# Performance work log

Hardware: AMD Instinct MI355X
Metric: run time of the kernel (lower is better)

Reference implementation:

```python
import jax, jax.numpy as jnp
import numpy as np

K0 = 0.7978845608028654  # sqrt(2/pi)
C1 = 0.044715

def _gelu_tanh(x):
    # tanh-approx GELU, matching the Triton kernel's math
    return 0.5 * x * (1.0 + jnp.tanh(K0 * (x + C1 * x * x * x)))

def setup_inputs() -> dict:
    key = jax.random.key(0)
    k1, k2, k3 = jax.random.split(key, 3)
    B, C_in, H, W = 32, 64, 128, 128
    C_out, KH = 128, 3
    x = jax.random.normal(k1, (B, C_in, H, W), dtype=jnp.float32)
    weight = jax.random.normal(k2, (C_out, C_in, KH, KH), dtype=jnp.float32)
    bias = jax.random.normal(k3, (C_out,), dtype=jnp.float32)
    return {"x": x, "weight": weight, "bias": bias}

def reference(x, weight, bias):
    # Valid conv2d, stride 1 (NCHW, OIHW)
    y = jax.lax.conv_general_dilated(
        x, weight,
        window_strides=(1, 1), padding="VALID",
        dimension_numbers=("NCHW", "OIHW", "NCHW"))
    y = y + bias[None, :, None, None]
    y = _gelu_tanh(y)
    # global average pool over spatial dims -> [B, C_out]
    return jnp.mean(y, axis=(2, 3))
```

## Files before the change

### kernel.cpp

```cpp
#include <hip/hip_runtime.h>
#include <cstdint>
#include <cstddef>

#define GK0 0.7978845608028654f
#define GC1 0.044715f

typedef __attribute__((ext_vector_type(8))) short short8;
typedef __attribute__((ext_vector_type(4))) float floatx4;

__device__ __forceinline__ unsigned short f2bf(float f) {
  union { float f; unsigned int u; } v; v.f = f;
  unsigned int r = v.u + 0x7fffu + ((v.u >> 16) & 1u);
  return (unsigned short)(r >> 16);
}

__global__ void k_wt(const float* __restrict__ w, unsigned short* __restrict__ wt) {
  int t = blockIdx.x * 256 + threadIdx.x;
  if (t >= 128 * 64 * 9) return;
  int co = t / 576; int r = t - co * 576; int ci = r / 9; int khw = r - ci * 9;
  wt[(khw * 128 + co) * 64 + ci] = f2bf(w[t]);
}

__global__ void k_xt(const float* __restrict__ x, unsigned short* __restrict__ xb) {
  __shared__ float tile[128 * 65];
  int b = blockIdx.y, h = blockIdx.x;
  const float* src = x + ((size_t)b * 64 * 128 + h) * 128;
  for (int i = threadIdx.x; i < 64 * 128; i += 256) {
    int ci = i >> 7, w = i & 127;
    tile[w * 65 + ci] = src[(size_t)ci * 16384 + w];
  }
  __syncthreads();
  uint32_t* dst = (uint32_t*)(xb + (((size_t)b * 128 + h) * 128) * 64);
  for (int i = threadIdx.x; i < 128 * 32; i += 256) {
    int w = i >> 5, c2 = (i & 31) << 1;
    uint32_t u0 = f2bf(tile[w * 65 + c2]);
    uint32_t u1 = f2bf(tile[w * 65 + c2 + 1]);
    dst[i] = u0 | (u1 << 16);
  }
}

__global__ __launch_bounds__(256) void k_conv(
    const unsigned short* __restrict__ xb, const unsigned short* __restrict__ wt,
    const float* __restrict__ bias, float* __restrict__ out) {
  __shared__ unsigned short xs[4 * 66 * 72];
  const int tid = threadIdx.x;
  const int b = blockIdx.z, h0 = blockIdx.y * 2, w0 = blockIdx.x * 64;

  {
    const size_t base = (((size_t)b * 128 + h0) * 128) * 64;
    for (int t = tid; t < 2112; t += 256) {
      int hi = t / 528; int rem = t - hi * 528; int wi = rem >> 3; int c8 = (rem & 7) << 3;
      int wg = w0 + wi;
      int4 val = make_int4(0, 0, 0, 0);
      if (wg < 128) val = *(const int4*)(xb + base + ((size_t)hi * 128 + wg) * 64 + c8);
      *(int4*)(&xs[(hi * 66 + wi) * 72 + c8]) = val;
    }
  }
  __syncthreads();

  const int lane = tid & 63, wave = tid >> 6;
  const int wm = wave & 1, wn = wave >> 1;
  const int m = lane & 15, q = lane >> 4;

  floatx4 acc[4][4];
#pragma unroll
  for (int i = 0; i < 4; i++)
#pragma unroll
    for (int j = 0; j < 4; j++) acc[i][j] = (floatx4){0.f, 0.f, 0.f, 0.f};

  const unsigned short* wbase = wt + ((wm * 64 + m) * 64 + q * 8);
  int bb[4];
#pragma unroll
  for (int nt = 0; nt < 4; nt++) bb[nt] = (wn * 66 + nt * 16 + m) * 72 + q * 8;

  short8 a_cur[4], a_nxt[4];
#pragma unroll
  for (int mt = 0; mt < 4; mt++) a_cur[mt] = *(const short8*)(wbase + mt * 1024);

#pragma unroll
  for (int kk = 0; kk < 18; kk++) {
    const int khw = kk >> 1, cb = (kk & 1) << 5;
    const int kh = khw / 3, kw = khw - kh * 3;
    if (kk < 17) {
      const int khw2 = (kk + 1) >> 1, cb2 = ((kk + 1) & 1) << 5;
      const unsigned short* p = wbase + khw2 * 8192 + cb2;
#pragma unroll
      for (int mt = 0; mt < 4; mt++) a_nxt[mt] = *(const short8*)(p + mt * 1024);
    }
    short8 bf[4];
    const int off = (kh * 66 + kw) * 72 + cb;
#pragma unroll
    for (int nt = 0; nt < 4; nt++) bf[nt] = *(const short8*)(&xs[bb[nt] + off]);
#pragma unroll
    for (int mt = 0; mt < 4; mt++)
#pragma unroll
      for (int nt = 0; nt < 4; nt++)
        acc[mt][nt] = __builtin_amdgcn_mfma_f32_16x16x32_bf16(a_cur[mt], bf[nt], acc[mt][nt], 0, 0, 0);
#pragma unroll
    for (int mt = 0; mt < 4; mt++) a_cur[mt] = a_nxt[mt];
  }

  const float inv_area = 1.0f / (126.0f * 126.0f);
  float* orow = out + b * 128;
#pragma unroll
  for (int mt = 0; mt < 4; mt++) {
#pragma unroll
    for (int r = 0; r < 4; r++) {
      const int co = wm * 64 + mt * 16 + q * 4 + r;
      const float bv = bias[co];
      float s = 0.0f;
#pragma unroll
      for (int nt = 0; nt < 4; nt++) {
        float y = acc[mt][nt][r] + bv;
        float u = GK0 * (y + GC1 * y * y * y);
        float g = 0.5f * y * (1.0f + tanhf(u));
        if (w0 + nt * 16 + m < 126) s += g;
      }
#pragma unroll
      for (int d = 1; d < 16; d <<= 1) s += __shfl_xor(s, d, 64);
      if (m == 0) atomicAdd(&orow[co], s * inv_area);
    }
  }
}

extern "C" void kernel_launch(void* const* d_in, const int* in_sizes, int n_in,
                              void* d_out, int out_size, void* d_ws, size_t ws_size,
                              hipStream_t stream) {
  const float* x    = (const float*)d_in[0];
  const float* w    = (const float*)d_in[1];
  const float* bias = (const float*)d_in[2];
  float* out = (float*)d_out;

  unsigned short* xbuf = (unsigned short*)d_ws;
  unsigned short* wbuf = xbuf + (size_t)32 * 128 * 128 * 64;
  if (ws_size < (size_t)32 * 128 * 128 * 64 * 2 + 73728 * 2) return;

  hipMemsetAsync(d_out, 0, (size_t)out_size * sizeof(float), stream);
  k_wt<<<288, 256, 0, stream>>>(w, wbuf);
  k_xt<<<dim3(128, 32), 256, 0, stream>>>(x, xbuf);
  k_conv<<<dim3(2, 63, 32), 256, 0, stream>>>(xbuf, wbuf, bias, out);
}
```

Measured before the change: 434.9 us.

## Fuse fp32-to-bf16 input conversion into conv kernel, drop transpose pass

Removes the separate layout-transpose kernel and its bf16 workspace buffer; the conv kernel now loads fp32 NCHW rows directly, converts to bf16 and scatters into channel-last shared memory. GELU's tanh is rewritten as a sigmoid via fast exp and reciprocal, and launch bounds request higher occupancy. This trades an extra global write/read pass for redundant overlapping row reads and strided 2-byte shared stores that may bank-conflict.

```diff
diff --git a/kernel.cpp b/kernel.cpp
--- a/kernel.cpp
+++ b/kernel.cpp
@@ -21,40 +21,28 @@
   wt[(khw * 128 + co) * 64 + ci] = f2bf(w[t]);
 }
 
-__global__ void k_xt(const float* __restrict__ x, unsigned short* __restrict__ xb) {
-  __shared__ float tile[128 * 65];
-  int b = blockIdx.y, h = blockIdx.x;
-  const float* src = x + ((size_t)b * 64 * 128 + h) * 128;
-  for (int i = threadIdx.x; i < 64 * 128; i += 256) {
-    int ci = i >> 7, w = i & 127;
-    tile[w * 65 + ci] = src[(size_t)ci * 16384 + w];
-  }
-  __syncthreads();
-  uint32_t* dst = (uint32_t*)(xb + (((size_t)b * 128 + h) * 128) * 64);
-  for (int i = threadIdx.x; i < 128 * 32; i += 256) {
-    int w = i >> 5, c2 = (i & 31) << 1;
-    uint32_t u0 = f2bf(tile[w * 65 + c2]);
-    uint32_t u1 = f2bf(tile[w * 65 + c2 + 1]);
-    dst[i] = u0 | (u1 << 16);
-  }
-}
-
-__global__ __launch_bounds__(256) void k_conv(
-    const unsigned short* __restrict__ xb, const unsigned short* __restrict__ wt,
+__global__ __launch_bounds__(256, 4) void k_conv(
+    const float* __restrict__ x, const unsigned short* __restrict__ wt,
     const float* __restrict__ bias, float* __restrict__ out) {
   __shared__ unsigned short xs[4 * 66 * 72];
   const int tid = threadIdx.x;
   const int b = blockIdx.z, h0 = blockIdx.y * 2, w0 = blockIdx.x * 64;
 
   {
-    const size_t base = (((size_t)b * 128 + h0) * 128) * 64;
-    for (int t = tid; t < 2112; t += 256) {
-      int hi = t / 528; int rem = t - hi * 528; int wi = rem >> 3; int c8 = (rem & 7) << 3;
-      int wg = w0 + wi;
-      int4 val = make_int4(0, 0, 0, 0);
-      if (wg < 128) val = *(const int4*)(xb + base + ((size_t)hi * 128 + wg) * 64 + c8);
-      *(int4*)(&xs[(hi * 66 + wi) * 72 + c8]) = val;
+    const int ci = tid >> 2, hi = tid & 3;
+    const float* src = x + ((size_t)(b * 64 + ci) * 128 + (h0 + hi)) * 128 + w0;
+    unsigned short* dst = xs + (hi * 66) * 72 + ci;
+#pragma unroll 4
+    for (int v = 0; v < 16; v++) {
+      float4 f = ((const float4*)src)[v];
+      dst[(4 * v + 0) * 72] = f2bf(f.x);
+      dst[(4 * v + 1) * 72] = f2bf(f.y);
+      dst[(4 * v + 2) * 72] = f2bf(f.z);
+      dst[(4 * v + 3) * 72] = f2bf(f.w);
     }
+    const bool ok = (w0 == 0);
+    dst[64 * 72] = ok ? f2bf(src[64]) : (unsigned short)0;
+    dst[65 * 72] = ok ? f2bf(src[65]) : (unsigned short)0;
   }
   __syncthreads();
 
@@ -113,7 +101,8 @@
       for (int nt = 0; nt < 4; nt++) {
         float y = acc[mt][nt][r] + bv;
         float u = GK0 * (y + GC1 * y * y * y);
-        float g = 0.5f * y * (1.0f + tanhf(u));
+        float e = __expf(-2.0f * u);
+        float g = y * __builtin_amdgcn_rcpf(1.0f + e);
         if (w0 + nt * 16 + m < 126) s += g;
       }
 #pragma unroll
@@ -131,12 +120,10 @@
   const float* bias = (const float*)d_in[2];
   float* out = (float*)d_out;
 
-  unsigned short* xbuf = (unsigned short*)d_ws;
-  unsigned short* wbuf = xbuf + (size_t)32 * 128 * 128 * 64;
-  if (ws_size < (size_t)32 * 128 * 128 * 64 * 2 + 73728 * 2) return;
+  unsigned short* wbuf = (unsigned short*)d_ws;
+  if (ws_size < (size_t)9 * 128 * 64 * 2) return;
 
   hipMemsetAsync(d_out, 0, (size_t)out_size * sizeof(float), stream);
   k_wt<<<288, 256, 0, stream>>>(w, wbuf);
-  k_xt<<<dim3(128, 32), 256, 0, stream>>>(x, xbuf);
-  k_conv<<<dim3(2, 63, 32), 256, 0, stream>>>(xbuf, wbuf, bias, out);
+  k_conv<<<dim3(2, 63, 32), 256, 0, stream>>>(x, wbuf, bias, out);
 }
```

Measured after the change: 397.9 us. 8.5% less time.
